# Kernel tuning notes

Measured on AMD Instinct MI355X. Metric: run time of the kernel, lower is better.

The kernel has to match this reference:

```python
import jax, jax.numpy as jnp
import numpy as np

D_MODEL = 1024
N_HEADS = 16
D_KEY = D_MODEL // N_HEADS
NEG = -1e9


def setup_inputs() -> dict:
    key = jax.random.key(0)
    ks = jax.random.split(key, 10)
    B, S = 4, 2048
    s = 0.02
    query = jax.random.normal(ks[0], (B, S, D_MODEL), dtype=jnp.float32)
    # causal mask: 1 where attend allowed, 0 where masked (masked_fill(mask==0, -1e9))
    mask = jnp.tril(jnp.ones((S, S), dtype=jnp.int32))[None, None]
    Wq = jax.random.normal(ks[1], (D_MODEL, D_MODEL), dtype=jnp.float32) * s
    bq = jax.random.normal(ks[2], (D_MODEL,), dtype=jnp.float32) * s
    Wk = jax.random.normal(ks[3], (D_MODEL, D_MODEL), dtype=jnp.float32) * s
    bk = jax.random.normal(ks[4], (D_MODEL,), dtype=jnp.float32) * s
    Wv = jax.random.normal(ks[5], (D_MODEL, D_MODEL), dtype=jnp.float32) * s
    bv = jax.random.normal(ks[6], (D_MODEL,), dtype=jnp.float32) * s
    Wo = jax.random.normal(ks[7], (D_MODEL, D_MODEL), dtype=jnp.float32) * s
    bo = jax.random.normal(ks[8], (D_MODEL,), dtype=jnp.float32) * s
    return {"query": query, "mask": mask, "Wq": Wq, "bq": bq, "Wk": Wk,
            "bk": bk, "Wv": Wv, "bv": bv, "Wo": Wo, "bo": bo}


def _split_heads(x):
    B, S, _ = x.shape
    return x.reshape(B, S, N_HEADS, D_KEY).transpose(0, 2, 1, 3)  # [B,H,S,Dk]


def reference(query, mask, Wq, bq, Wk, bk, Wv, bv, Wo, bo):
    B, S, _ = query.shape
    # torch Linear: x @ W^T + b
    q = _split_heads(query @ Wq.T + bq)
    k = _split_heads(query @ Wk.T + bk)  # self-attention: key_value is None
    v = _split_heads(query @ Wv.T + bv)
    scores = jnp.einsum('bhqd,bhkd->bhqk', q, k) / jnp.sqrt(jnp.float32(D_KEY))
    scores = jnp.where(mask == 0, jnp.float32(NEG), scores)
    weights = jax.nn.softmax(scores, axis=-1)  # dropout=0 (eval)
    attn = jnp.einsum('bhqk,bhkd->bhqd', weights, v)
    merged = attn.transpose(0, 2, 1, 3).reshape(B, S, D_MODEL)
    return merged @ Wo.T + bo
```

## Files before the change

### kernel.cpp

```cpp
#include <hip/hip_runtime.h>
#include <hip/hip_bf16.h>

typedef __attribute__((ext_vector_type(8))) short bf16x8;
typedef __attribute__((ext_vector_type(4))) float f32x4;
typedef __attribute__((ext_vector_type(16))) float f32x16;
typedef __attribute__((ext_vector_type(2))) unsigned int u32x2;

__device__ __forceinline__ float fexp2(float x) { return __builtin_amdgcn_exp2f(x); }

__device__ __forceinline__ ushort f2bf(float x) {
    union { float f; unsigned u; } c; c.f = x;
    unsigned r = c.u + 0x7fff + ((c.u >> 16) & 1);
    return (ushort)(r >> 16);
}

__device__ __forceinline__ unsigned cvtpk(float lo, float hi) {
    unsigned r;
    asm("v_cvt_pk_bf16_f32 %0, %1, %2" : "=v"(r) : "v"(lo), "v"(hi));
    return r;
}

__device__ __forceinline__ void gload16(const void* g, void* l) {
    __builtin_amdgcn_global_load_lds((const __attribute__((address_space(1))) void*)g,
                                     (__attribute__((address_space(3))) void*)l, 16, 0, 0);
}

__device__ __forceinline__ void blockbar() {
    asm volatile("" ::: "memory");
    __builtin_amdgcn_s_barrier();
    asm volatile("" ::: "memory");
}

__global__ void cvt_f32_bf16(const float* __restrict__ in, ushort* __restrict__ out, int n4) {
    int i = blockIdx.x * blockDim.x + threadIdx.x;
    int stride = gridDim.x * blockDim.x;
    for (; i < n4; i += stride) {
        float4 v = ((const float4*)in)[i];
        ushort4 o;
        o.x = f2bf(v.x); o.y = f2bf(v.y); o.z = f2bf(v.z); o.w = f2bf(v.w);
        ((ushort4*)out)[i] = o;
    }
}

__global__ void cvt_w4(const float* __restrict__ a, const float* __restrict__ b,
                       const float* __restrict__ c, const float* __restrict__ d,
                       ushort* __restrict__ oq, ushort* __restrict__ ow) {
    const int N4 = 262144;
    int i = blockIdx.x * blockDim.x + threadIdx.x;
    int stride = gridDim.x * blockDim.x;
    for (; i < 4 * N4; i += stride) {
        int sel = i >> 18, local = i & (N4 - 1);
        const float* src = (sel == 0) ? a : (sel == 1) ? b : (sel == 2) ? c : d;
        float4 v = ((const float4*)src)[local];
        ushort4 o;
        o.x = f2bf(v.x); o.y = f2bf(v.y); o.z = f2bf(v.z); o.w = f2bf(v.w);
        if (sel < 3) ((ushort4*)oq)[sel * N4 + local] = o;
        else         ((ushort4*)ow)[local] = o;
    }
}

template<int MODE>
__global__ __launch_bounds__(256)
void gemm_m97(const ushort* __restrict__ A, const ushort* __restrict__ Bt,
              const float* __restrict__ bias0, const float* __restrict__ bias1,
              const float* __restrict__ bias2,
              ushort* __restrict__ outb, float* __restrict__ outf,
              int M, int N, int K) {
    __shared__ ushort As[128 * 32];
    __shared__ ushort Bs[128 * 32];
    const int t = threadIdx.x, lane = t & 63, w = t >> 6;
    const int wr = w >> 1, wc = w & 1;
    const int l15 = lane & 15, lg = lane >> 4;
    const int nwg = gridDim.x * gridDim.y;
    const int bid = blockIdx.y * gridDim.x + blockIdx.x;
    const int swz = (bid & 7) * (nwg >> 3) + (bid >> 3);
    const int m0 = (swz / gridDim.x) * 128, n0 = (swz % gridDim.x) * 128;
    const int srow = lane >> 2;
    const int sg = (lane & 3) ^ ((lane >> 2) & 3);

    f32x4 acc[4][4] = {};

    for (int k0 = 0; k0 < K; k0 += 32) {
#pragma unroll
        for (int i = 0; i < 2; i++) {
            int c = i * 4 + w;
            const ushort* as = A + (size_t)(m0 + c * 16 + srow) * K + k0 + sg * 8;
            const ushort* bs = Bt + (size_t)(n0 + c * 16 + srow) * K + k0 + sg * 8;
            gload16(as, &As[c * 512]);
            gload16(bs, &Bs[c * 512]);
        }
        __syncthreads();
        bf16x8 af[4], bfr[4];
#pragma unroll
        for (int mi = 0; mi < 4; mi++) {
            int row = wr * 64 + mi * 16 + l15;
            af[mi] = *(const bf16x8*)&As[row * 32 + ((lg ^ (row & 3)) << 3)];
        }
#pragma unroll
        for (int ni = 0; ni < 4; ni++) {
            int row = wc * 64 + ni * 16 + l15;
            bfr[ni] = *(const bf16x8*)&Bs[row * 32 + ((lg ^ (row & 3)) << 3)];
        }
        __builtin_amdgcn_s_setprio(1);
#pragma unroll
        for (int mi = 0; mi < 4; mi++)
#pragma unroll
            for (int ni = 0; ni < 4; ni++)
                acc[mi][ni] = __builtin_amdgcn_mfma_f32_16x16x32_bf16(af[mi], bfr[ni], acc[mi][ni], 0, 0, 0);
        __builtin_amdgcn_s_setprio(0);
        __syncthreads();
    }

#pragma unroll
    for (int mi = 0; mi < 4; mi++)
#pragma unroll
        for (int ni = 0; ni < 4; ni++)
#pragma unroll
            for (int r = 0; r < 4; r++) {
                int gm = m0 + wr * 64 + mi * 16 + lg * 4 + r;
                int gn = n0 + wc * 64 + ni * 16 + l15;
                if (MODE == 0) {
                    const float* bp = (gn < 1024) ? bias0 : ((gn < 2048) ? bias1 : bias2);
                    float v = acc[mi][ni][r] + bp[gn & 1023];
                    if (gn < 1024) v *= 0.18033688011f;
                    int proj = gn >> 10, nn = gn & 1023;
                    int h = nn >> 6, d = nn & 63;
                    int b = gm >> 11, s = gm & 2047;
                    outb[(size_t)proj * 8388608 + ((((size_t)b << 4) + h) * 2048 + s) * 64 + d] = f2bf(v);
                } else {
                    outf[(size_t)gm * N + gn] = acc[mi][ni][r] + bias0[gn];
                }
            }
}

__global__ __launch_bounds__(256, 3)
void attn_fwd(const ushort* __restrict__ Qb, const ushort* __restrict__ Kb,
              const ushort* __restrict__ Vb, ushort* __restrict__ Ab) {
    constexpr int S = 2048;
    __shared__ ushort lds[16384];

    const int bid = blockIdx.x;
    const int qt = 15 - (bid >> 6);
    const int bh = bid & 63;
    const int b = bh >> 4, h = bh & 15;
    const ushort* Qp = Qb + (size_t)bh * S * 64;
    const ushort* Kp = Kb + (size_t)bh * S * 64;
    const ushort* Vp = Vb + (size_t)bh * S * 64;

    const int t = threadIdx.x, lane = t & 63, w = t >> 6;
    const int l15 = lane & 15, l31 = lane & 31, hi = lane >> 5, g = lane >> 4;

    int koff[2], voff[2];
#pragma unroll
    for (int i = 0; i < 2; i++) {
        int row = (w * 2 + i) * 8 + (lane >> 3);
        int gg = (lane & 7) ^ ((row ^ (row >> 3)) & 7);
        koff[i] = row * 64 + gg * 8;
    }
#pragma unroll
    for (int it = 0; it < 2; it++) {
        int T = (it * 4 + w) * 64 + lane;
        int kvb = T >> 5, db = (T >> 3) & 3, kvr = (T >> 1) & 3, dh = T & 1;
        voff[it] = (kvb * 4 + kvr) * 64 + db * 16 + dh * 8;
    }
    const unsigned vtbase = (unsigned)(uintptr_t)&lds[8192]
                          + (hi << 10) + ((g & 1) << 7) + (l15 << 3);

    auto stage = [&](int phase, int k0) {
#pragma unroll
        for (int i = 0; i < 2; i++)
            gload16(Kp + (size_t)k0 * 64 + koff[i], &lds[(phase << 12) + ((w * 2 + i) << 9)]);
#pragma unroll
        for (int it = 0; it < 2; it++)
            gload16(Vp + (size_t)k0 * 64 + voff[it], &lds[8192 + (phase << 12) + (((it << 2) + w) << 9)]);
    };

    const int fb = qt * 128 + w * 32;
    const int nt = 2 * qt + 2;

    bf16x8 qf[4];
#pragma unroll
    for (int kc = 0; kc < 4; kc++)
        qf[kc] = *(const bf16x8*)&Qp[(size_t)(fb + l31) * 64 + kc * 16 + hi * 8];

    float m = -3e38f, ls = 0.f;
    f32x16 O0 = {}, O1 = {};

    stage(0, 0);

    for (int tile = 0; tile < nt; tile++) {
        const int phase = tile & 1;
        const int k0 = tile * 64;
        if (tile + 1 < nt) {
            stage(phase ^ 1, (tile + 1) * 64);
            asm volatile("s_waitcnt vmcnt(4)" ::: "memory");
        } else {
            asm volatile("s_waitcnt vmcnt(0)" ::: "memory");
        }
        blockbar();

        if (k0 <= fb + 31) {
            const ushort* Kc = &lds[phase << 12];
            f32x16 s0 = {}, s1 = {};
            {
                bf16x8 kf[4];
#pragma unroll
                for (int kc = 0; kc < 4; kc++) {
                    int row = l31;
                    int sw = (row ^ (row >> 3)) & 7;
                    kf[kc] = *(const bf16x8*)&Kc[row * 64 + (((kc * 2 + hi) ^ sw) << 3)];
                }
                __builtin_amdgcn_s_setprio(1);
#pragma unroll
                for (int kc = 0; kc < 4; kc++)
                    s0 = __builtin_amdgcn_mfma_f32_32x32x16_bf16(kf[kc], qf[kc], s0, 0, 0, 0);
                __builtin_amdgcn_s_setprio(0);
            }
            {
                bf16x8 kf[4];
#pragma unroll
                for (int kc = 0; kc < 4; kc++) {
                    int row = 32 + l31;
                    int sw = (row ^ (row >> 3)) & 7;
                    kf[kc] = *(const bf16x8*)&Kc[row * 64 + (((kc * 2 + hi) ^ sw) << 3)];
                }
                __builtin_amdgcn_s_setprio(1);
#pragma unroll
                for (int kc = 0; kc < 4; kc++)
                    s1 = __builtin_amdgcn_mfma_f32_32x32x16_bf16(kf[kc], qf[kc], s1, 0, 0, 0);
                __builtin_amdgcn_s_setprio(0);
            }

            float pv[32];
            const bool diag = (k0 + 63 > fb);
            const int rel = fb + l31 - k0 - 4 * hi;
#pragma unroll
            for (int r = 0; r < 16; r++) {
                float v0 = s0[r], v1 = s1[r];
                if (diag) {
                    int kvc = (r & 3) + 8 * (r >> 2);
                    if (kvc > rel)      v0 = -1e30f;
                    if (kvc + 32 > rel) v1 = -1e30f;
                }
                pv[r] = v0; pv[16 + r] = v1;
            }
            float mx[16];
#pragma unroll
            for (int i = 0; i < 16; i++) mx[i] = fmaxf(pv[i], pv[i + 16]);
#pragma unroll
            for (int sgap = 8; sgap >= 1; sgap >>= 1)
#pragma unroll
                for (int i = 0; i < sgap; i++) mx[i] = fmaxf(mx[i], mx[i + sgap]);
            float pmax = fmaxf(mx[0], __shfl_xor(mx[0], 32));

            if (!__all(pmax <= m + 8.f)) {
                float mnew = fmaxf(m, pmax);
                float a = fexp2(m - mnew);
                ls *= a;
                float ar[16];
#pragma unroll
                for (int r = 0; r < 16; r++)
                    ar[r] = __shfl(a, (r & 3) + 8 * (r >> 2) + 4 * hi, 32);
#pragma unroll
                for (int r = 0; r < 16; r++) { O0[r] *= ar[r]; O1[r] *= ar[r]; }
                m = mnew;
            }
#pragma unroll
            for (int i = 0; i < 32; i++) pv[i] = fexp2(pv[i] - m);
            float sm[16];
#pragma unroll
            for (int i = 0; i < 16; i++) sm[i] = pv[i] + pv[i + 16];
#pragma unroll
            for (int sgap = 8; sgap >= 1; sgap >>= 1)
#pragma unroll
                for (int i = 0; i < sgap; i++) sm[i] += sm[i + sgap];
            ls += sm[0] + __shfl_xor(sm[0], 32);

            union PAu { bf16x8 v; unsigned wd[4]; } PA[4];
#pragma unroll
            for (int ks = 0; ks < 4; ks++)
#pragma unroll
                for (int i = 0; i < 2; i++) {
                    unsigned xw = cvtpk(pv[8 * ks + 2 * i], pv[8 * ks + 2 * i + 1]);
                    unsigned yw = cvtpk(pv[8 * ks + 2 * i + 4], pv[8 * ks + 2 * i + 5]);
                    asm("v_permlane32_swap_b32 %0, %1" : "+v"(xw), "+v"(yw));
                    PA[ks].wd[i] = xw; PA[ks].wd[2 + i] = yw;
                }

            const unsigned vtb = vtbase + (phase << 13);
            u32x2 vb[16];
#define TRR(idx, OFFSTR) asm volatile("ds_read_b64_tr_b16 %0, %1 offset:" OFFSTR : "=v"(vb[idx]) : "v"(vtb))
            TRR(0, "0");    TRR(1, "512");  TRR(2, "2048"); TRR(3, "2560");
            TRR(4, "4096"); TRR(5, "4608"); TRR(6, "6144"); TRR(7, "6656");
            TRR(8, "256");  TRR(9, "768");  TRR(10, "2304"); TRR(11, "2816");
            TRR(12, "4352"); TRR(13, "4864"); TRR(14, "6400"); TRR(15, "6912");
#undef TRR
            union FragU { bf16x8 v; u32x2 hh[2]; };
            asm volatile("s_waitcnt lgkmcnt(8)" ::: "memory");
            __builtin_amdgcn_sched_barrier(0);
            __builtin_amdgcn_s_setprio(1);
#pragma unroll
            for (int ks = 0; ks < 4; ks++) {
                FragU f; f.hh[0] = vb[ks * 2]; f.hh[1] = vb[ks * 2 + 1];
                O0 = __builtin_amdgcn_mfma_f32_32x32x16_bf16(PA[ks].v, f.v, O0, 0, 0, 0);
            }
            __builtin_amdgcn_s_setprio(0);
            asm volatile("s_waitcnt lgkmcnt(0)" ::: "memory");
            __builtin_amdgcn_sched_barrier(0);
            __builtin_amdgcn_s_setprio(1);
#pragma unroll
            for (int ks = 0; ks < 4; ks++) {
                FragU f; f.hh[0] = vb[8 + ks * 2]; f.hh[1] = vb[8 + ks * 2 + 1];
                O1 = __builtin_amdgcn_mfma_f32_32x32x16_bf16(PA[ks].v, f.v, O1, 0, 0, 0);
            }
            __builtin_amdgcn_s_setprio(0);
        }
        blockbar();
    }

    float inv[16];
#pragma unroll
    for (int r = 0; r < 16; r++)
        inv[r] = __builtin_amdgcn_rcpf(__shfl(ls, (r & 3) + 8 * (r >> 2) + 4 * hi, 32));
#pragma unroll
    for (int r = 0; r < 16; r++) {
        int q = fb + (r & 3) + 8 * (r >> 2) + 4 * hi;
        size_t base = ((size_t)b * 2048 + q) * 1024 + h * 64;
        Ab[base + l31]      = f2bf(O0[r] * inv[r]);
        Ab[base + 32 + l31] = f2bf(O1[r] * inv[r]);
    }
}

extern "C" void kernel_launch(void* const* d_in, const int* in_sizes, int n_in,
                              void* d_out, int out_size, void* d_ws, size_t ws_size,
                              hipStream_t stream) {
    const float* query = (const float*)d_in[0];
    const float* Wq = (const float*)d_in[2];
    const float* bq = (const float*)d_in[3];
    const float* Wk = (const float*)d_in[4];
    const float* bk = (const float*)d_in[5];
    const float* Wv = (const float*)d_in[6];
    const float* bv = (const float*)d_in[7];
    const float* Wo = (const float*)d_in[8];
    const float* bo = (const float*)d_in[9];
    float* out = (float*)d_out;

    char* ws = (char*)d_ws;
    const size_t SZ_X = 8192ull * 1024 * 2;
    const size_t SZ_W = 1024ull * 1024 * 2;
    ushort* Xb   = (ushort*)(ws);
    ushort* Wcat = (ushort*)(ws + SZ_X);
    ushort* Wob  = (ushort*)(ws + SZ_X + 3 * SZ_W);
    ushort* QKVb = (ushort*)(ws + SZ_X + 4 * SZ_W);
    ushort* Ab   = (ushort*)(ws + 4 * SZ_X + 4 * SZ_W);

    cvt_f32_bf16<<<1024, 256, 0, stream>>>(query, Xb, 8192 * 1024 / 4);
    cvt_w4<<<1024, 256, 0, stream>>>(Wq, Wk, Wv, Wo, Wcat, Wob);

    gemm_m97<0><<<dim3(3072 / 128, 8192 / 128), 256, 0, stream>>>(
        Xb, Wcat, bq, bk, bv, QKVb, nullptr, 8192, 3072, 1024);

    attn_fwd<<<1024, 256, 0, stream>>>(QKVb, QKVb + 8388608, QKVb + 2 * 8388608, Ab);

    gemm_m97<1><<<dim3(1024 / 128, 8192 / 128), 256, 0, stream>>>(
        Ab, Wob, bo, nullptr, nullptr, nullptr, out, 8192, 1024, 1024);
}
```

Measured before the change: 175.1 us.

## Rewrite projection GEMMs with 256x128 tiles, 8 waves and 4-stage LDS pipeline

New measurement: 174.6 us. About the same (-0.3%).

```diff
diff --git a/kernel.cpp b/kernel.cpp
--- a/kernel.cpp
+++ b/kernel.cpp
@@ -29,6 +29,13 @@
     asm volatile("" ::: "memory");
     __builtin_amdgcn_s_barrier();
     asm volatile("" ::: "memory");
+}
+
+template<int N> __device__ __forceinline__ void vmwait() {
+    if constexpr (N == 9)      asm volatile("s_waitcnt vmcnt(9)" ::: "memory");
+    else if constexpr (N == 6) asm volatile("s_waitcnt vmcnt(6)" ::: "memory");
+    else if constexpr (N == 3) asm volatile("s_waitcnt vmcnt(3)" ::: "memory");
+    else                       asm volatile("s_waitcnt vmcnt(0)" ::: "memory");
 }
 
 __global__ void cvt_f32_bf16(const float* __restrict__ in, ushort* __restrict__ out, int n4) {
@@ -60,47 +67,63 @@
 }
 
 template<int MODE>
-__global__ __launch_bounds__(256)
-void gemm_m97(const ushort* __restrict__ A, const ushort* __restrict__ Bt,
-              const float* __restrict__ bias0, const float* __restrict__ bias1,
-              const float* __restrict__ bias2,
-              ushort* __restrict__ outb, float* __restrict__ outf,
-              int M, int N, int K) {
-    __shared__ ushort As[128 * 32];
-    __shared__ ushort Bs[128 * 32];
+__global__ __launch_bounds__(512, 2)
+void gemm_8p(const ushort* __restrict__ A, const ushort* __restrict__ Bt,
+             const float* __restrict__ bias0, const float* __restrict__ bias1,
+             const float* __restrict__ bias2,
+             ushort* __restrict__ outb, float* __restrict__ outf,
+             int M, int N, int K) {
+    __shared__ ushort lds[49152];
     const int t = threadIdx.x, lane = t & 63, w = t >> 6;
-    const int wr = w >> 1, wc = w & 1;
+    const int wm = w >> 1, wn = w & 1;
     const int l15 = lane & 15, lg = lane >> 4;
-    const int nwg = gridDim.x * gridDim.y;
-    const int bid = blockIdx.y * gridDim.x + blockIdx.x;
+    const int asw = (l15 >> 1) & 3;
+
+    const int nbx = N >> 7;
+    const int nwg = nbx * (M >> 8);
+    const int bid = blockIdx.y * nbx + blockIdx.x;
     const int swz = (bid & 7) * (nwg >> 3) + (bid >> 3);
-    const int m0 = (swz / gridDim.x) * 128, n0 = (swz % gridDim.x) * 128;
+    const int m0 = (swz / nbx) * 256, n0 = (swz % nbx) * 128;
+
     const int srow = lane >> 2;
-    const int sg = (lane & 3) ^ ((lane >> 2) & 3);
+    const int sblk = (lane & 3) ^ ((lane >> 3) & 3);
+    const ushort* Asrc0 = A + (size_t)(m0 + 16 * w + srow) * K + sblk * 8;
+    const ushort* Asrc1 = A + (size_t)(m0 + 128 + 16 * w + srow) * K + sblk * 8;
+    const ushort* Bsrc  = Bt + (size_t)(n0 + 16 * w + srow) * K + sblk * 8;
+    ushort* ldsA0 = &lds[w * 512];
+    ushort* ldsA1 = &lds[(8 + w) * 512];
+    ushort* ldsB  = &lds[8192 + w * 512];
+
+#define STAGE(ST, KT) { \
+    gload16(Asrc0 + (KT) * 32, ldsA0 + (ST) * 12288); \
+    gload16(Asrc1 + (KT) * 32, ldsA1 + (ST) * 12288); \
+    gload16(Bsrc  + (KT) * 32, ldsB  + (ST) * 12288); }
+
+    const int abase = (wm * 64 + l15) * 32 + ((lg ^ asw) << 3);
+    const int bbase = 8192 + (wn * 64 + l15) * 32 + ((lg ^ asw) << 3);
 
     f32x4 acc[4][4] = {};
-
-    for (int k0 = 0; k0 < K; k0 += 32) {
-#pragma unroll
-        for (int i = 0; i < 2; i++) {
-            int c = i * 4 + w;
-            const ushort* as = A + (size_t)(m0 + c * 16 + srow) * K + k0 + sg * 8;
-            const ushort* bs = Bt + (size_t)(n0 + c * 16 + srow) * K + k0 + sg * 8;
-            gload16(as, &As[c * 512]);
-            gload16(bs, &Bs[c * 512]);
-        }
-        __syncthreads();
+    const int NT = K >> 5;
+
+    STAGE(0, 0); STAGE(1, 1); STAGE(2, 2);
+
+    for (int kt = 0; kt < NT; ++kt) {
+        if (kt + 3 < NT) STAGE((kt + 3) & 3, kt + 3);
+        const int ahead = NT - 1 - kt;
+        if (ahead >= 3) vmwait<9>();
+        else if (ahead == 2) vmwait<6>();
+        else if (ahead == 1) vmwait<3>();
+        else vmwait<0>();
+        blockbar();
+
+        const ushort* sa = lds + (kt & 3) * 12288 + abase;
+        const ushort* sb = lds + (kt & 3) * 12288 + bbase;
         bf16x8 af[4], bfr[4];
 #pragma unroll
-        for (int mi = 0; mi < 4; mi++) {
-            int row = wr * 64 + mi * 16 + l15;
-            af[mi] = *(const bf16x8*)&As[row * 32 + ((lg ^ (row & 3)) << 3)];
-        }
-#pragma unroll
-        for (int ni = 0; ni < 4; ni++) {
-            int row = wc * 64 + ni * 16 + l15;
-            bfr[ni] = *(const bf16x8*)&Bs[row * 32 + ((lg ^ (row & 3)) << 3)];
-        }
+        for (int mi = 0; mi < 4; mi++) af[mi] = *(const bf16x8*)(sa + mi * 512);
+#pragma unroll
+        for (int ni = 0; ni < 4; ni++) bfr[ni] = *(const bf16x8*)(sb + ni * 512);
+
         __builtin_amdgcn_s_setprio(1);
 #pragma unroll
         for (int mi = 0; mi < 4; mi++)
@@ -108,8 +131,9 @@
             for (int ni = 0; ni < 4; ni++)
                 acc[mi][ni] = __builtin_amdgcn_mfma_f32_16x16x32_bf16(af[mi], bfr[ni], acc[mi][ni], 0, 0, 0);
         __builtin_amdgcn_s_setprio(0);
-        __syncthreads();
-    }
+        blockbar();
+    }
+#undef STAGE
 
 #pragma unroll
     for (int mi = 0; mi < 4; mi++)
@@ -117,8 +141,8 @@
         for (int ni = 0; ni < 4; ni++)
 #pragma unroll
             for (int r = 0; r < 4; r++) {
-                int gm = m0 + wr * 64 + mi * 16 + lg * 4 + r;
-                int gn = n0 + wc * 64 + ni * 16 + l15;
+                int gm = m0 + wm * 64 + mi * 16 + lg * 4 + r;
+                int gn = n0 + wn * 64 + ni * 16 + l15;
                 if (MODE == 0) {
                     const float* bp = (gn < 1024) ? bias0 : ((gn < 2048) ? bias1 : bias2);
                     float v = acc[mi][ni][r] + bp[gn & 1023];
@@ -357,11 +381,11 @@
     cvt_f32_bf16<<<1024, 256, 0, stream>>>(query, Xb, 8192 * 1024 / 4);
     cvt_w4<<<1024, 256, 0, stream>>>(Wq, Wk, Wv, Wo, Wcat, Wob);
 
-    gemm_m97<0><<<dim3(3072 / 128, 8192 / 128), 256, 0, stream>>>(
+    gemm_8p<0><<<dim3(3072 / 128, 8192 / 256), 512, 0, stream>>>(
         Xb, Wcat, bq, bk, bv, QKVb, nullptr, 8192, 3072, 1024);
 
     attn_fwd<<<1024, 256, 0, stream>>>(QKVb, QKVb + 8388608, QKVb + 2 * 8388608, Ab);
 
-    gemm_m97<1><<<dim3(1024 / 128, 8192 / 128), 256, 0, stream>>>(
+    gemm_8p<1><<<dim3(1024 / 128, 8192 / 256), 512, 0, stream>>>(
         Ab, Wob, bo, nullptr, nullptr, nullptr, out, 8192, 1024, 1024);
 }
```
